# Kernel optimization log

Measured on AMD Instinct MI355X. Metric: run time of the kernel, lower is better.

The kernel has to match this reference:

```python
import jax, jax.numpy as jnp
import numpy as np
import math

DIM = 1024      # dim == dim_attn (required by value-reshape)
HEAD = 16
KV = 128        # K_v routing slots
HD = DIM // HEAD
N = 50000       # number of nodes


def setup_inputs() -> dict:
    key = jax.random.key(0)
    ks = jax.random.split(key, 8)
    s = lambda fan_in: 1.0 / np.sqrt(fan_in)
    return {
        "x": jax.random.normal(ks[0], (N, DIM), jnp.float32),
        "node_index": jax.random.normal(ks[1], (N, 4), jnp.float32),
        # nn.Linear(dim, dim_attn)
        "Wq": jax.random.normal(ks[2], (DIM, DIM), jnp.float32) * s(DIM),
        "bq": jnp.zeros((DIM,), jnp.float32),
        # nn.Parameter key (K_v, head, head_dim), torch.randn init
        "key_p": jax.random.normal(ks[3], (KV, HEAD, HD), jnp.float32),
        # nn.Linear(dim, dim)
        "Wv": jax.random.normal(ks[4], (DIM, DIM), jnp.float32) * s(DIM),
        "bv": jnp.zeros((DIM,), jnp.float32),
        # gate params, shape (head, 1)
        "alpha": jnp.full((HEAD, 1), math.log(9.0), jnp.float32),
        "beta": jnp.full((HEAD, 1), math.log(0.01), jnp.float32),
        # nn.Linear(4, head*K_v)
        "Wb": jax.random.normal(ks[5], (HEAD * KV, 4), jnp.float32) * s(4),
        "bb": jnp.zeros((HEAD * KV,), jnp.float32),
    }


def _mh_sinkhorn(A, num_iters=3, eps=0.05):
    # A: (N, H, K). Faithful to the per-head torch sinkhorn (Q transposed to
    # (K, N)): row sums are over the node axis, col sums over the slot axis.
    n = A.shape[0]
    k = A.shape[2]
    Q = jnp.exp(A / eps)
    Q = Q / jnp.sum(Q, axis=(0, 2), keepdims=True)          # total-sum norm per head
    for _ in range(num_iters):
        Q = Q / jnp.sum(Q, axis=0, keepdims=True) / k       # rows of Q.T (per slot)
        Q = Q / jnp.sum(Q, axis=2, keepdims=True) / n       # cols of Q.T (per node)
    return Q * n


def reference(x, node_index, Wq, bq, key_p, Wv, bv, alpha, beta, Wb, bb):
    n = x.shape[0]
    q = (x @ Wq.T + bq).reshape(n, HEAD, HD)
    attn = jnp.einsum('nhd,rhd->nhr', q, key_p) / np.float32(np.sqrt(HD))
    bias = (node_index @ Wb.T + bb).reshape(n, HEAD, KV)
    attn = attn + bias                                       # (n, H, K_v)
    xv = (x @ Wv.T + bv).reshape(n, HEAD, HD)
    v = jnp.einsum('nhr,nhd->rhd', jax.nn.sigmoid(attn), xv)  # (K_v, H, D)
    cons = _mh_sinkhorn(jax.nn.softmax(attn, axis=-1))
    v = jnp.einsum('nhr,rhd->nhd', cons, v)
    out = jax.nn.sigmoid(alpha) * xv + jax.nn.sigmoid(beta) * v  # (H,1) broadcasts
    return out.reshape(n, DIM)
```

## Files before the change

kernel.cpp:

```cpp
#include <hip/hip_runtime.h>

#define N_NODES 50000
#define MPAD    50176
#define DIM     1024
#define HEAD    16
#define KV      128
#define HD      64
#define NGRP    98

typedef unsigned short ushort_t;
typedef short short8 __attribute__((ext_vector_type(8)));
typedef float f32x4 __attribute__((ext_vector_type(4)));

__device__ inline unsigned short f2bf(float f){
  union { float f; unsigned u; } v; v.f = f;
  unsigned u = v.u;
  unsigned r = (u + 0x7FFFu + ((u >> 16) & 1u)) >> 16;
  return (unsigned short)r;
}
__device__ inline float bf2f(unsigned short u){
  union { unsigned u; float f; } v; v.u = ((unsigned)u) << 16; return v.f;
}

__device__ inline void gload_lds16(const void* g, void* l){
  __builtin_amdgcn_global_load_lds(
      (const __attribute__((address_space(1))) void*)g,
      (__attribute__((address_space(3))) void*)l, 16, 0, 0);
}

__device__ inline short8 frag64(const ushort_t* lds, int row, int kk, int lane){
  int c  = kk*4 + (lane >> 4);
  int cc = c ^ (row & 7);
  return *(const short8*)(lds + row*64 + cc*8);
}
__device__ inline short8 frag128(const ushort_t* lds, int row, int kk, int lane){
  int c  = kk*4 + (lane >> 4);
  int cc = c ^ (row & 7);
  return *(const short8*)(lds + row*128 + cc*8);
}

__global__ void k_zero(float* p, int n){
  int i = blockIdx.x*256 + threadIdx.x;
  if (i < n) p[i] = 0.f;
}

__global__ void k_prep_x(const float* __restrict__ x, ushort_t* __restrict__ x_bf){
  int idx = blockIdx.x*256 + threadIdx.x;
  int row = idx >> 7, c = idx & 127;
  const float4* s = (const float4*)(x + (size_t)row*1024 + c*8);
  float4 f0 = s[0], f1 = s[1];
  short8 v;
  v[0]=(short)f2bf(f0.x); v[1]=(short)f2bf(f0.y); v[2]=(short)f2bf(f0.z); v[3]=(short)f2bf(f0.w);
  v[4]=(short)f2bf(f1.x); v[5]=(short)f2bf(f1.y); v[6]=(short)f2bf(f1.z); v[7]=(short)f2bf(f1.w);
  int sc = (c & ~3) | ((c ^ (row >> 1)) & 3);
  *(short8*)(x_bf + (size_t)row*1024 + sc*8) = v;
}

__global__ void k_prep_w(const float* __restrict__ Wq, const float* __restrict__ Wv,
                         ushort_t* __restrict__ w_bf){
  int idx = blockIdx.x*256 + threadIdx.x;
  int j = idx >> 10, k = idx & 1023;
  float v = (j < 1024) ? Wq[idx] : Wv[(size_t)(j-1024)*1024 + k];
  int l = k >> 3;
  int q = (l & ~3) | ((l ^ (j >> 1)) & 3);
  w_bf[(size_t)j*1024 + q*8 + (k & 7)] = f2bf(v);
}

__global__ void k_prep_key(const float* __restrict__ key_p, ushort_t* __restrict__ key_bf){
  int idx = blockIdx.x*256 + threadIdx.x;
  int h = idx >> 13, rem = idx & 8191;
  int r = rem >> 6, d = rem & 63;
  float v = key_p[(size_t)(r*HEAD + h)*HD + d];
  int pos = ((((d>>3) ^ (r & 7)) & 7) << 3) | (d & 7);
  key_bf[(size_t)h*8192 + r*64 + pos] = f2bf(v);
}

__global__ void k_vreduce(const float* __restrict__ vp, float* __restrict__ vout){
  int i = blockIdx.x*256 + threadIdx.x;
  float s = 0.f;
  for (int gg = 0; gg < NGRP; ++gg) s += vp[(size_t)gg*131072 + i];
  vout[i] = s;
}

__global__ __launch_bounds__(512) void k_gemm(const ushort_t* __restrict__ x_bf,
    const ushort_t* __restrict__ w_bf, const float* __restrict__ bq,
    const float* __restrict__ bv, ushort_t* __restrict__ q_bf, float* xv_out){
  extern __shared__ char gsm[];
  ushort_t* lds = (ushort_t*)gsm;
  const int tid = threadIdx.x, lane = tid & 63;
  const int wid = tid >> 6, wr = wid >> 2, wc = wid & 3;
  int b = blockIdx.x;
  int wg = (b & 7)*196 + (b >> 3);
  const int bm0 = (wg >> 3) * 256, bn0 = (wg & 7) * 256;
  const int pA = (lane >> 4) ^ ((lane >> 1) & 3);

  f32x4 acc[8][4];
  #pragma unroll
  for (int m=0;m<8;m++)
    #pragma unroll
    for (int n=0;n<4;n++) acc[m][n] = (f32x4){0.f,0.f,0.f,0.f};

  const ushort_t* asrc = x_bf + (size_t)bm0*1024;
  const ushort_t* bsrc = w_bf + (size_t)bn0*1024;

#define STG(kt, kk, bi) do{                                               \
    _Pragma("unroll")                                                     \
    for (int it=0; it<2; ++it){                                           \
      int ch = it*512 + tid; int r = ch>>2, c = ch&3;                     \
      gload_lds16(asrc + (size_t)r*1024 + (kt)*64 + (kk)*32 + c*8,        \
                  lds + (bi)*32768 + (kk)*8192 + ch*8);                   \
      gload_lds16(bsrc + (size_t)r*1024 + (kt)*64 + (kk)*32 + c*8,        \
                  lds + (bi)*32768 + 16384 + (kk)*8192 + ch*8);           \
    } }while(0)

#define RD_A(BASE, KK, MH)                                                \
    _Pragma("unroll")                                                     \
    for (int m=0;m<4;m++){                                                \
      int row = wr*128 + ((MH)*4+m)*16 + (lane&15);                       \
      af[m] = *(const short8*)((BASE) + (KK)*8192 + row*32 + pA*8);       \
    }
#define RD_B(BASE, KK)                                                    \
    _Pragma("unroll")                                                     \
    for (int n=0;n<4;n++){                                                \
      int row = wc*64 + n*16 + (lane&15);                                 \
      bf_[n] = *(const short8*)((BASE) + 16384 + (KK)*8192 + row*32 + pA*8); \
    }
#define MFMA16(MH)                                                        \
    __builtin_amdgcn_s_setprio(1);                                        \
    _Pragma("unroll")                                                     \
    for (int m=0;m<4;m++)                                                 \
      _Pragma("unroll")                                                   \
      for (int n=0;n<4;n++)                                               \
        acc[(MH)*4+m][n] = __builtin_amdgcn_mfma_f32_16x16x32_bf16(       \
            af[m], bf_[n], acc[(MH)*4+m][n], 0,0,0);                      \
    __builtin_amdgcn_s_setprio(0);
#define BAR asm volatile("s_barrier" ::: "memory")

  STG(0,0,0); STG(0,1,0); STG(1,0,1);
  asm volatile("s_waitcnt vmcnt(8)" ::: "memory");
  BAR;

  for (int t = 0; t < 16; ++t){
    const int bufc = t & 1, bufn = bufc ^ 1;
    const ushort_t* base = lds + bufc*32768;
    short8 af[4], bf_[4];

    RD_B(base, 0);
    RD_A(base, 0, 0);
    if (t+1 < 16) STG(t+1, 1, bufn);
    BAR;
    MFMA16(0);
    BAR;

    RD_A(base, 0, 1);
    BAR;
    MFMA16(1);
    if (t == 15) { asm volatile("s_waitcnt vmcnt(0)" ::: "memory"); }
    else         { asm volatile("s_waitcnt vmcnt(8)" ::: "memory"); }
    BAR;

    RD_B(base, 1);
    RD_A(base, 1, 0);
    if (t+2 < 16) STG(t+2, 0, bufc);
    BAR;
    MFMA16(0);
    BAR;

    RD_A(base, 1, 1);
    BAR;
    MFMA16(1);
    if (t <= 13)      { asm volatile("s_waitcnt vmcnt(8)" ::: "memory"); }
    else if (t == 14) { asm volatile("s_waitcnt vmcnt(4)" ::: "memory"); }
    BAR;
  }
#undef STG
#undef RD_A
#undef RD_B
#undef MFMA16
#undef BAR

  __syncthreads();

  const bool isq = bn0 < 1024;
  float biasv[4];
  #pragma unroll
  for (int n=0;n<4;n++){
    int col = bn0 + wc*64 + n*16 + (lane & 15);
    biasv[n] = isq ? bq[col] : bv[col - 1024];
  }

  if (isq){
    ushort_t* img = (ushort_t*)gsm;
    #pragma unroll
    for (int n=0;n<4;n++){
      int lcol = wc*64 + n*16 + (lane & 15);
      int d = lcol & 63;
      #pragma unroll
      for (int m=0;m<8;m++){
        #pragma unroll
        for (int j=0;j<4;j++){
          int lrow = wr*128 + m*16 + (lane>>4)*4 + j;
          int sc = (lcol & ~63) | ((((d>>3) ^ (lrow & 7)) & 7) << 3) | (d & 7);
          img[lrow*256 + sc] = f2bf(acc[m][n][j] + biasv[n]);
        }
      }
    }
    __syncthreads();
    #pragma unroll
    for (int it=0; it<16; ++it){
      int r  = it*16 + (tid >> 5);
      int ch = tid & 31;
      short8 v = *(const short8*)(img + r*256 + ch*8);
      *(short8*)(q_bf + (size_t)(bm0 + r)*1024 + bn0 + ch*8) = v;
    }
  } else {
    #pragma unroll
    for (int n=0;n<4;n++){
      int col = bn0 + wc*64 + n*16 + (lane & 15);
      #pragma unroll
      for (int m=0;m<8;m++){
        #pragma unroll
        for (int j=0;j<4;j++){
          int row = bm0 + wr*128 + m*16 + (lane>>4)*4 + j;
          if (row < N_NODES)
            xv_out[(size_t)row*1024 + (col - 1024)] = acc[m][n][j] + biasv[n];
        }
      }
    }
  }
}

template<int PHASE>
__global__ __launch_bounds__(256) void k_attn(
    const ushort_t* __restrict__ q_bf, const ushort_t* __restrict__ key_bf,
    const float* __restrict__ node_index, const float* __restrict__ Wb,
    const float* __restrict__ bb, const float* __restrict__ colsum_in,
    float* __restrict__ colsum_out, const float* __restrict__ v_fin,
    float* __restrict__ v_part, float* xv_out,
    const float* __restrict__ alpha, const float* __restrict__ beta)
{
  constexpr int QB    = (PHASE == 2) ? 1 : 2;
  constexpr int O_Q   = 0;
  constexpr int O_KEY = O_Q + QB*8192;
  constexpr int O_NI  = O_KEY + 16384;
  constexpr int O_WB  = O_NI + QB*1024;
  constexpr int O_RED = O_WB + 2560;
  constexpr int O_COL = O_RED + 2048;
  constexpr int O_W   = O_COL + 512;
  constexpr int O_X1  = O_W + 512;
  constexpr int O_X2  = O_X1 + 16384;

  extern __shared__ char smem[];
  ushort_t* q_lds   = (ushort_t*)(smem + O_Q);
  ushort_t* key_lds = (ushort_t*)(smem + O_KEY);
  float* ni_lds  = (float*)(smem + O_NI);
  float* wb_lds  = (float*)(smem + O_WB);
  float* red_lds = (float*)(smem + O_RED);
  float* col_acc = (float*)(smem + O_COL);
  float* w_lds   = (float*)(smem + O_W);
  ushort_t* sigT     = (ushort_t*)(smem + O_X1);
  ushort_t* xvT      = (ushort_t*)(smem + O_X2);
  ushort_t* vT       = (ushort_t*)(smem + O_X1);
  ushort_t* cons_lds = (ushort_t*)(smem + O_X2);
  float*    out_lds  = (float*)(smem + O_X2);

  const int tid = threadIdx.x, lane = tid & 63, wid = tid >> 6;
  const int h    = blockIdx.x & 15;
  const int g    = blockIdx.x >> 4;
  const int base = g * 512;
  int NT = (MPAD - base) >> 6; if (NT > 8) NT = 8;

  #pragma unroll
  for (int it = 0; it < 4; ++it){
    int chunk = it*256 + tid;
    gload_lds16(key_bf + (size_t)h*8192 + chunk*8, key_lds + chunk*8);
  }
  #pragma unroll
  for (int it = 0; it < 2; ++it){
    int chunk = it*256 + tid;
    int r = chunk >> 3, c = chunk & 7;
    gload_lds16(q_bf + (size_t)(base + r)*1024 + h*64 + c*8, q_lds + chunk*8);
  }
  { int r = tid >> 2, c = tid & 3;
    ni_lds[tid] = (base + r < N_NODES) ? node_index[(size_t)(base + r)*4 + c] : 0.f; }
  if (tid < 128){
    #pragma unroll
    for (int c=0;c<4;c++) wb_lds[tid*5+c] = Wb[(size_t)(h*128 + tid)*4 + c];
    wb_lds[tid*5+4] = bb[h*128 + tid];
    if (PHASE >= 1) w_lds[tid] = 1.f / (128.f * colsum_in[h*128 + tid]);
    if (PHASE <= 1) col_acc[tid] = 0.f;
  }
  if constexpr (PHASE == 2){
    int r = tid >> 1, dh = (tid & 1)*32;
    #pragma unroll
    for (int i=0;i<32;i++){
      int d = dh + i;
      vT[d*128 + ((r>>3) ^ (d&7))*8 + (r&7)] = f2bf(v_fin[((size_t)r*16 + h)*64 + d]);
    }
  }
  float xvr[16], xvn[16];
  if constexpr (PHASE == 0){
    int d = tid & 63, q4 = tid >> 6;
    #pragma unroll
    for (int i=0;i<16;i++){
      int row = base + q4*16 + i;
      xvr[i] = (row < N_NODES) ? xv_out[(size_t)row*1024 + h*64 + d] : 0.f;
    }
  }
  f32x4 vac[2][4];
  if constexpr (PHASE == 0)
    for (int m=0;m<2;m++) for (int n=0;n<4;n++) vac[m][n] = (f32x4){0.f,0.f,0.f,0.f};

  __syncthreads();

  for (int t = 0; t < NT; ++t){
    const int i0  = base + t*64;
    const int cur = t & 1;
    const ushort_t* qb  = q_lds  + ((QB==2) ? cur*4096 : 0);
    const float*    nib = ni_lds + ((QB==2) ? cur*256  : 0);
    float ni_next = 0.f;

    if constexpr (QB == 2){
      if (t+1 < NT){
        int i1 = i0 + 64;
        #pragma unroll
        for (int it = 0; it < 2; ++it){
          int chunk = it*256 + tid;
          int r = chunk >> 3, c = chunk & 7;
          gload_lds16(q_bf + (size_t)(i1 + r)*1024 + h*64 + c*8,
                      q_lds + (cur^1)*4096 + chunk*8);
        }
        int r = tid >> 2, c = tid & 3;
        ni_next = (i0 + 64 + r < N_NODES) ? node_index[(size_t)(i0+64+r)*4 + c] : 0.f;
      }
    } else {
      if (t+1 < NT){
        int r = tid >> 2, c = tid & 3;
        ni_next = (i0 + 64 + r < N_NODES) ? node_index[(size_t)(i0+64+r)*4 + c] : 0.f;
      }
    }
    if constexpr (PHASE == 0){
      if (t+1 < NT){
        int d = tid & 63, q4 = tid >> 6;
        #pragma unroll
        for (int i=0;i<16;i++){
          int row = i0 + 64 + q4*16 + i;
          xvn[i] = (row < N_NODES) ? xv_out[(size_t)row*1024 + h*64 + d] : 0.f;
        }
      }
    }

    f32x4 acc[2][4];
    for (int m=0;m<2;m++) for (int n=0;n<4;n++) acc[m][n] = (f32x4){0.f,0.f,0.f,0.f};
    #pragma unroll
    for (int kk = 0; kk < 2; ++kk){
      short8 kf[2];
      #pragma unroll
      for (int m=0;m<2;m++) kf[m] = frag64(key_lds, wid*32 + m*16 + (lane&15), kk, lane);
      #pragma unroll
      for (int n=0;n<4;n++){
        short8 qf = frag64(qb, n*16 + (lane&15), kk, lane);
        #pragma unroll
        for (int m=0;m<2;m++)
          acc[m][n] = __builtin_amdgcn_mfma_f32_16x16x32_bf16(kf[m], qf, acc[m][n], 0,0,0);
      }
    }

    float nif[4][4];
    #pragma unroll
    for (int n=0;n<4;n++){
      int nn = n*16 + (lane&15);
      #pragma unroll
      for (int c=0;c<4;c++) nif[n][c] = nib[nn*4+c];
    }
    float a[2][4][4];
    #pragma unroll
    for (int m=0;m<2;m++){
      #pragma unroll
      for (int j=0;j<4;j++){
        int r = wid*32 + m*16 + (lane>>4)*4 + j;
        float w0 = wb_lds[r*5+0], w1 = wb_lds[r*5+1];
        float w2 = wb_lds[r*5+2], w3 = wb_lds[r*5+3], w4 = wb_lds[r*5+4];
        #pragma unroll
        for (int n=0;n<4;n++){
          float b = w4 + w0*nif[n][0] + w1*nif[n][1] + w2*nif[n][2] + w3*nif[n][3];
          a[m][n][j] = acc[m][n][j]*0.125f + b;
        }
      }
    }

    float vmask[4];
    #pragma unroll
    for (int n=0;n<4;n++) vmask[n] = (i0 + n*16 + (lane&15) < N_NODES) ? 1.f : 0.f;

    if constexpr (PHASE == 0){
      #pragma unroll
      for (int m=0;m<2;m++) for (int n=0;n<4;n++) for (int j=0;j<4;j++){
        int r  = wid*32 + m*16 + (lane>>4)*4 + j;
        int nn = n*16 + (lane&15);
        float sg = vmask[n] / (1.f + __expf(-a[m][n][j]));
        sigT[r*64 + ((((nn>>3) ^ (r&7)) & 7) << 3) + (nn&7)] = f2bf(sg);
      }
      { int d = tid & 63, q4 = tid >> 6;
        #pragma unroll
        for (int i=0;i<16;i++){
          int nn = q4*16 + i;
          xvT[d*64 + ((((nn>>3) ^ (d&7)) & 7) << 3) + (nn&7)] = f2bf(xvr[i]);
        }
      }
    }

    float pm[4];
    #pragma unroll
    for (int n=0;n<4;n++){
      float m0 = a[0][n][0];
      #pragma unroll
      for (int m=0;m<2;m++) for (int j=0;j<4;j++) m0 = fmaxf(m0, a[m][n][j]);
      m0 = fmaxf(m0, __shfl_xor(m0, 16));
      m0 = fmaxf(m0, __shfl_xor(m0, 32));
      pm[n] = m0;
    }
    if (lane < 16){
      #pragma unroll
      for (int n=0;n<4;n++) red_lds[wid*64 + n*16 + lane] = pm[n];
    }
    __syncthreads();

    if constexpr (QB == 1){
      if (t+1 < NT){
        int i1 = i0 + 64;
        #pragma unroll
        for (int it = 0; it < 2; ++it){
          int chunk = it*256 + tid;
          int r = chunk >> 3, c = chunk & 7;
          gload_lds16(q_bf + (size_t)(i1 + r)*1024 + h*64 + c*8, q_lds + chunk*8);
        }
        ni_lds[tid] = ni_next;
      }
    }

    float mnn[4], snn[4];
    #pragma unroll
    for (int n=0;n<4;n++){
      int nn = n*16 + (lane&15);
      float m0 = red_lds[nn];
      m0 = fmaxf(m0, red_lds[64+nn]); m0 = fmaxf(m0, red_lds[128+nn]); m0 = fmaxf(m0, red_lds[192+nn]);
      mnn[n] = m0;
    }
    #pragma unroll
    for (int n=0;n<4;n++){
      float s = 0.f;
      #pragma unroll
      for (int m=0;m<2;m++) for (int j=0;j<4;j++){
        float e = __expf(a[m][n][j] - mnn[n]);
        a[m][n][j] = e; s += e;
      }
      s += __shfl_xor(s, 16); s += __shfl_xor(s, 32);
      snn[n] = s;
    }
    if (lane < 16){
      #pragma unroll
      for (int n=0;n<4;n++) red_lds[256 + wid*64 + n*16 + lane] = snn[n];
    }

    if constexpr (PHASE == 0){
      #pragma unroll
      for (int kk=0;kk<2;kk++){
        short8 sa[2];
        #pragma unroll
        for (int m=0;m<2;m++) sa[m] = frag64(sigT, wid*32 + m*16 + (lane&15), kk, lane);
        #pragma unroll
        for (int n=0;n<4;n++){
          short8 xf = frag64(xvT, n*16 + (lane&15), kk, lane);
          #pragma unroll
          for (int m=0;m<2;m++)
            vac[m][n] = __builtin_amdgcn_mfma_f32_16x16x32_bf16(sa[m], xf, vac[m][n], 0,0,0);
        }
      }
    }
    __syncthreads();

    #pragma unroll
    for (int n=0;n<4;n++){
      int nn = n*16 + (lane&15);
      snn[n] = red_lds[256+nn] + red_lds[256+64+nn] + red_lds[256+128+nn] + red_lds[256+192+nn];
    }
    #pragma unroll
    for (int n=0;n<4;n++){
      float inv = 20.f / snn[n];
      #pragma unroll
      for (int m=0;m<2;m++) for (int j=0;j<4;j++)
        a[m][n][j] = __expf(a[m][n][j] * inv);
    }

    float uval[4];
    if constexpr (PHASE >= 1){
      #pragma unroll
      for (int n=0;n<4;n++){
        float s = 0.f;
        #pragma unroll
        for (int m=0;m<2;m++){
          #pragma unroll
          for (int j=0;j<4;j++){
            int r = wid*32 + m*16 + (lane>>4)*4 + j;
            s += a[m][n][j] * w_lds[r];
          }
        }
        s += __shfl_xor(s, 16); s += __shfl_xor(s, 32);
        uval[n] = s;
      }
      if (lane < 16){
        #pragma unroll
        for (int n=0;n<4;n++) red_lds[wid*64 + n*16 + lane] = uval[n];
      }
      __syncthreads();
      #pragma unroll
      for (int n=0;n<4;n++){
        int nn = n*16 + (lane&15);
        float s = red_lds[nn] + red_lds[64+nn] + red_lds[128+nn] + red_lds[192+nn];
        uval[n] = 1.f / (50000.f * s);
      }
    }

    if constexpr (PHASE <= 1){
      float cs[2][4];
      #pragma unroll
      for (int m=0;m<2;m++){
        #pragma unroll
        for (int j=0;j<4;j++){
          float s = 0.f;
          #pragma unroll
          for (int n=0;n<4;n++){
            float tv = a[m][n][j] * vmask[n];
            if (PHASE == 1) tv *= uval[n];
            s += tv;
          }
          s += __shfl_xor(s, 1); s += __shfl_xor(s, 2);
          s += __shfl_xor(s, 4); s += __shfl_xor(s, 8);
          cs[m][j] = s;
        }
      }
      if ((lane & 15) == 0){
        #pragma unroll
        for (int m=0;m<2;m++) for (int j=0;j<4;j++){
          int r = wid*32 + m*16 + (lane>>4)*4 + j;
          col_acc[r] += cs[m][j];
        }
      }
    }

    if constexpr (PHASE == 2){
      #pragma unroll
      for (int m=0;m<2;m++) for (int n=0;n<4;n++) for (int j=0;j<4;j++){
        int r  = wid*32 + m*16 + (lane>>4)*4 + j;
        int nn = n*16 + (lane&15);
        float cv = 50000.f * uval[n] * a[m][n][j] * w_lds[r];
        cons_lds[nn*128 + ((r>>3) ^ (nn&7))*8 + (r&7)] = f2bf(cv);
      }
      __syncthreads();
      f32x4 oac[4];
      for (int n=0;n<4;n++) oac[n] = (f32x4){0.f,0.f,0.f,0.f};
      #pragma unroll
      for (int kk=0;kk<4;kk++){
        short8 va = frag128(vT, wid*16 + (lane&15), kk, lane);
        #pragma unroll
        for (int n=0;n<4;n++){
          short8 cf = frag128(cons_lds, n*16 + (lane&15), kk, lane);
          oac[n] = __builtin_amdgcn_mfma_f32_16x16x32_bf16(va, cf, oac[n], 0,0,0);
        }
      }
      __syncthreads();
      #pragma unroll
      for (int n=0;n<4;n++) for (int j=0;j<4;j++){
        int d  = wid*16 + (lane>>4)*4 + j;
        int nn = n*16 + (lane&15);
        out_lds[nn*68 + d] = oac[n][j];
      }
      __syncthreads();
      float sa = 1.f/(1.f + __expf(-alpha[h]));
      float sb = 1.f/(1.f + __expf(-beta[h]));
      int nn = tid >> 2, d0 = (tid & 3)*16;
      if (i0 + nn < N_NODES){
        #pragma unroll
        for (int gq=0; gq<4; ++gq){
          float4 vf = *(const float4*)(out_lds + nn*68 + d0 + gq*4);
          float4 xf = *(const float4*)(xv_out + (size_t)(i0+nn)*1024 + h*64 + d0 + gq*4);
          float4 o;
          o.x = sa*xf.x + sb*vf.x;
          o.y = sa*xf.y + sb*vf.y;
          o.z = sa*xf.z + sb*vf.z;
          o.w = sa*xf.w + sb*vf.w;
          *(float4*)(xv_out + (size_t)(i0+nn)*1024 + h*64 + d0 + gq*4) = o;
        }
      }
    } else {
      if (t+1 < NT && QB == 2) ni_lds[(cur^1)*256 + tid] = ni_next;
      if constexpr (PHASE == 0){
        if (t+1 < NT){
          #pragma unroll
          for (int i=0;i<16;i++) xvr[i] = xvn[i];
        }
      }
      __syncthreads();
    }
  }

  if constexpr (PHASE == 0){
    float* vdst = v_part + (size_t)g*131072;
    #pragma unroll
    for (int m=0;m<2;m++) for (int n=0;n<4;n++) for (int j=0;j<4;j++){
      int r = wid*32 + m*16 + (lane>>4)*4 + j;
      int d = n*16 + (lane&15);
      vdst[((size_t)r*16 + h)*64 + d] = vac[m][n][j];
    }
  }
  if constexpr (PHASE <= 1){
    if (tid < 128) atomicAdd(&colsum_out[h*128 + tid], col_acc[tid]);
  }
}

extern "C" void kernel_launch(void* const* d_in, const int* in_sizes, int n_in,
                              void* d_out, int out_size, void* d_ws, size_t ws_size,
                              hipStream_t stream){
  const float* x     = (const float*)d_in[0];
  const float* ni    = (const float*)d_in[1];
  const float* Wq    = (const float*)d_in[2];
  const float* bq    = (const float*)d_in[3];
  const float* keyp  = (const float*)d_in[4];
  const float* Wv    = (const float*)d_in[5];
  const float* bv    = (const float*)d_in[6];
  const float* alpha = (const float*)d_in[7];
  const float* beta  = (const float*)d_in[8];
  const float* Wb    = (const float*)d_in[9];
  const float* bb    = (const float*)d_in[10];
  float* out = (float*)d_out;

  char* ws = (char*)d_ws;
  ushort_t* x_bf   = (ushort_t*)(ws);
  float*    v_part = (float*)(ws);
  ushort_t* q_bf   = (ushort_t*)(ws + 102760448);
  ushort_t* w_bf   = (ushort_t*)(ws + 205520896);
  ushort_t* key_bf = (ushort_t*)(ws + 209715200);
  float*    v_fin  = (float*)(ws + 209977344);
  float*    cs     = (float*)(ws + 210501632);

  (void)hipFuncSetAttribute((const void*)k_gemm,
      hipFuncAttributeMaxDynamicSharedMemorySize, 131072);

  k_zero<<<dim3(24), 256, 0, stream>>>(cs, 6144);
  k_zero<<<dim3(352), 256, 0, stream>>>((float*)(x_bf + (size_t)N_NODES*1024), 90112);
  k_prep_x<<<dim3(25000), 256, 0, stream>>>(x, x_bf);
  k_prep_w<<<dim3(2048*1024/256), 256, 0, stream>>>(Wq, Wv, w_bf);
  k_prep_key<<<dim3(HEAD*KV*HD/256), 256, 0, stream>>>(keyp, key_bf);
  k_gemm<<<dim3(1568), 512, 131072, stream>>>(x_bf, w_bf, bq, bv, q_bf, out);

  dim3 ag(NGRP*16);
  k_attn<0><<<ag, 256, 65024, stream>>>(q_bf, key_bf, ni, Wb, bb, nullptr,  cs,      v_fin, v_part, out, alpha, beta);
  k_vreduce<<<dim3(512), 256, 0, stream>>>(v_part, v_fin);
  k_attn<1><<<ag, 256, 40448, stream>>>(q_bf, key_bf, ni, Wb, bb, cs,       cs+2048, v_fin, v_part, out, alpha, beta);
  k_attn<1><<<ag, 256, 40448, stream>>>(q_bf, key_bf, ni, Wb, bb, cs+2048,  cs+4096, v_fin, v_part, out, alpha, beta);
  k_attn<2><<<ag, 256, 65024, stream>>>(q_bf, key_bf, ni, Wb, bb, cs+4096,  nullptr, v_fin, v_part, out, alpha, beta);
}
```

Measured before the change: 951.0 us.

## Materialize exp-softmax tiles once and run Sinkhorn passes from cached bf16 tiles

Phase 0 of the attention kernel now writes the per-node exponentiated Sinkhorn input Q0 to workspace in bf16. Two lightweight kernels then read these tiles for the column-sum iterations, and a final kernel does the consensus matmul and output blend. This avoids recomputing the q·key products, bias and exp in every Sinkhorn phase. The cost is extra workspace traffic of about 200MB per pass and bf16 rounding of Q0. The old path is kept as a fallback when the workspace is too small.

New measurement: 1.135 ms. 19.3% more time.

```diff
diff --git a/kernel.cpp b/kernel.cpp
--- a/kernel.cpp
+++ b/kernel.cpp
@@ -7,6 +7,7 @@
 #define KV      128
 #define HD      64
 #define NGRP    98
+#define NTILE   784
 
 typedef unsigned short ushort_t;
 typedef short short8 __attribute__((ext_vector_type(8)));
@@ -18,8 +19,8 @@
   unsigned r = (u + 0x7FFFu + ((u >> 16) & 1u)) >> 16;
   return (unsigned short)r;
 }
-__device__ inline float bf2f(unsigned short u){
-  union { unsigned u; float f; } v; v.u = ((unsigned)u) << 16; return v.f;
+__device__ inline float bf2f(unsigned u16){
+  union { unsigned u; float f; } v; v.u = (u16 & 0xFFFFu) << 16; return v.f;
 }
 
 __device__ inline void gload_lds16(const void* g, void* l){
@@ -237,7 +238,8 @@
     const float* __restrict__ bb, const float* __restrict__ colsum_in,
     float* __restrict__ colsum_out, const float* __restrict__ v_fin,
     float* __restrict__ v_part, float* xv_out,
-    const float* __restrict__ alpha, const float* __restrict__ beta)
+    const float* __restrict__ alpha, const float* __restrict__ beta,
+    ushort_t* __restrict__ q0g)
 {
   constexpr int QB    = (PHASE == 2) ? 1 : 2;
   constexpr int O_Q   = 0;
@@ -493,6 +495,19 @@
         a[m][n][j] = __expf(a[m][n][j] * inv);
     }
 
+    if constexpr (PHASE == 0){
+      if (q0g){
+        size_t ub = (size_t)((i0 >> 6)*16 + h) * 8192;
+        #pragma unroll
+        for (int m=0;m<2;m++) for (int n=0;n<4;n++){
+          uint2 pv;
+          pv.x = (unsigned)f2bf(a[m][n][0]) | ((unsigned)f2bf(a[m][n][1]) << 16);
+          pv.y = (unsigned)f2bf(a[m][n][2]) | ((unsigned)f2bf(a[m][n][3]) << 16);
+          *(uint2*)(q0g + ub + ((size_t)((wid*2+m)*4 + n))*256 + lane*4) = pv;
+        }
+      }
+    }
+
     float uval[4];
     if constexpr (PHASE >= 1){
       #pragma unroll
@@ -616,6 +631,172 @@
   }
   if constexpr (PHASE <= 1){
     if (tid < 128) atomicAdd(&colsum_out[h*128 + tid], col_acc[tid]);
+  }
+}
+
+__global__ __launch_bounds__(256) void k_p1(const ushort_t* __restrict__ q0g,
+    const float* __restrict__ cs_in, float* __restrict__ cs_out){
+  const int tid = threadIdx.x, lane = tid & 63, wid = tid >> 6;
+  const int gw = blockIdx.x*4 + wid;
+  const int rg = lane >> 4, ln = lane & 15;
+  #pragma unroll 1
+  for (int it = 0; it < 4; ++it){
+    int unit = gw*4 + it;
+    int T = unit >> 4, h = unit & 15;
+    const ushort_t* ubase = q0g + (size_t)unit*8192;
+    float wv[8][4];
+    #pragma unroll
+    for (int a2=0;a2<8;a2++){
+      float4 c4 = *(const float4*)(cs_in + h*128 + a2*16 + rg*4);
+      wv[a2][0] = 1.f/(128.f*c4.x); wv[a2][1] = 1.f/(128.f*c4.y);
+      wv[a2][2] = 1.f/(128.f*c4.z); wv[a2][3] = 1.f/(128.f*c4.w);
+    }
+    float up[4] = {0.f,0.f,0.f,0.f};
+    #pragma unroll
+    for (int f=0; f<32; f++){
+      uint2 d = *(const uint2*)(ubase + (size_t)f*256 + lane*4);
+      int a2 = f>>2, n = f&3;
+      up[n] += bf2f(d.x)*wv[a2][0] + bf2f(d.x>>16)*wv[a2][1]
+             + bf2f(d.y)*wv[a2][2] + bf2f(d.y>>16)*wv[a2][3];
+    }
+    float msk[4];
+    #pragma unroll
+    for (int n=0;n<4;n++){
+      float s = up[n];
+      s += __shfl_xor(s,16); s += __shfl_xor(s,32);
+      float uu = 1.f/(50000.f*s);
+      msk[n] = (T*64 + n*16 + ln < N_NODES) ? uu : 0.f;
+    }
+    float ca[32];
+    #pragma unroll
+    for (int s5=0;s5<32;s5++) ca[s5] = 0.f;
+    #pragma unroll
+    for (int f=0; f<32; f++){
+      uint2 d = *(const uint2*)(ubase + (size_t)f*256 + lane*4);
+      int a2 = f>>2, n = f&3;
+      ca[a2*4+0] += msk[n]*bf2f(d.x);
+      ca[a2*4+1] += msk[n]*bf2f(d.x>>16);
+      ca[a2*4+2] += msk[n]*bf2f(d.y);
+      ca[a2*4+3] += msk[n]*bf2f(d.y>>16);
+    }
+    #pragma unroll
+    for (int s5=0;s5<32;s5++){
+      float v = ca[s5];
+      v += __shfl_xor(v,1); v += __shfl_xor(v,2);
+      v += __shfl_xor(v,4); v += __shfl_xor(v,8);
+      ca[s5] = v;
+    }
+    if (ln == 0){
+      #pragma unroll
+      for (int s5=0;s5<32;s5++){
+        int r = (s5>>2)*16 + rg*4 + (s5&3);
+        atomicAdd(&cs_out[h*128 + r], ca[s5]);
+      }
+    }
+  }
+}
+
+__global__ __launch_bounds__(256) void k_p2(const ushort_t* __restrict__ q0g,
+    const float* __restrict__ cs_in, const float* __restrict__ v_fin,
+    float* xv_out, const float* __restrict__ alpha, const float* __restrict__ beta){
+  __shared__ ushort_t vT[64*128];
+  __shared__ float X2[64*68];
+  __shared__ float w_lds[128];
+  __shared__ float red_lds[256];
+  ushort_t* cons_lds = (ushort_t*)X2;
+  float* out_lds = X2;
+
+  const int tid = threadIdx.x, lane = tid & 63, wid = tid >> 6;
+  const int h = blockIdx.x & 15;
+  const int g = blockIdx.x >> 4;
+  const int nn = tid & 63, rq = tid >> 6;
+
+  { int r = tid >> 1, dh = (tid & 1)*32;
+    #pragma unroll
+    for (int i=0;i<32;i++){
+      int d = dh + i;
+      vT[d*128 + ((r>>3) ^ (d&7))*8 + (r&7)] = f2bf(v_fin[((size_t)r*16 + h)*64 + d]);
+    } }
+  if (tid < 128) w_lds[tid] = 1.f/(128.f * cs_in[h*128 + tid]);
+  __syncthreads();
+
+  const float sa = 1.f/(1.f + __expf(-alpha[h]));
+  const float sb = 1.f/(1.f + __expf(-beta[h]));
+
+  for (int t = 0; t < 8; ++t){
+    const int i0 = g*512 + t*64;
+    const int T  = g*8 + t;
+    const ushort_t* ubase = q0g + (size_t)(T*16 + h)*8192;
+
+    float q0v[2][4][4], wreg[2][4][4];
+    float up = 0.f;
+    #pragma unroll
+    for (int m=0;m<2;m++){
+      #pragma unroll
+      for (int rg=0;rg<4;rg++){
+        uint2 d = *(const uint2*)(ubase + (size_t)((rq*2+m)*4 + (nn>>4)))*0 +
+                  *(const uint2*)(ubase + ((size_t)((rq*2+m)*4 + (nn>>4)))*256 + (rg*16 + (nn&15))*4);
+        float4 w4 = *(const float4*)(w_lds + rq*32 + m*16 + rg*4);
+        q0v[m][rg][0] = bf2f(d.x);     wreg[m][rg][0] = w4.x;
+        q0v[m][rg][1] = bf2f(d.x>>16); wreg[m][rg][1] = w4.y;
+        q0v[m][rg][2] = bf2f(d.y);     wreg[m][rg][2] = w4.z;
+        q0v[m][rg][3] = bf2f(d.y>>16); wreg[m][rg][3] = w4.w;
+        #pragma unroll
+        for (int j=0;j<4;j++) up += q0v[m][rg][j]*wreg[m][rg][j];
+      }
+    }
+    red_lds[rq*64 + nn] = up;
+    __syncthreads();
+    float u3 = 1.f/(50000.f*(red_lds[nn] + red_lds[64+nn] + red_lds[128+nn] + red_lds[192+nn]));
+    float scale = 50000.f * u3;
+    #pragma unroll
+    for (int m=0;m<2;m++){
+      #pragma unroll
+      for (int rg=0;rg<4;rg++){
+        int r0 = rq*32 + m*16 + rg*4;
+        unsigned lo = (unsigned)f2bf(scale*q0v[m][rg][0]*wreg[m][rg][0])
+                    | ((unsigned)f2bf(scale*q0v[m][rg][1]*wreg[m][rg][1]) << 16);
+        unsigned hi = (unsigned)f2bf(scale*q0v[m][rg][2]*wreg[m][rg][2])
+                    | ((unsigned)f2bf(scale*q0v[m][rg][3]*wreg[m][rg][3]) << 16);
+        uint2 pv; pv.x = lo; pv.y = hi;
+        *(uint2*)(cons_lds + nn*128 + ((r0>>3) ^ (nn&7))*8 + (r0&7)) = pv;
+      }
+    }
+    __syncthreads();
+    f32x4 oac[4];
+    for (int n=0;n<4;n++) oac[n] = (f32x4){0.f,0.f,0.f,0.f};
+    #pragma unroll
+    for (int kk=0;kk<4;kk++){
+      short8 va = frag128(vT, wid*16 + (lane&15), kk, lane);
+      #pragma unroll
+      for (int n=0;n<4;n++){
+        short8 cf = frag128(cons_lds, n*16 + (lane&15), kk, lane);
+        oac[n] = __builtin_amdgcn_mfma_f32_16x16x32_bf16(va, cf, oac[n], 0,0,0);
+      }
+    }
+    __syncthreads();
+    #pragma unroll
+    for (int n=0;n<4;n++) for (int j=0;j<4;j++){
+      int d  = wid*16 + (lane>>4)*4 + j;
+      int n2 = n*16 + (lane&15);
+      out_lds[n2*68 + d] = oac[n][j];
+    }
+    __syncthreads();
+    { int n2 = tid >> 2, d0 = (tid & 3)*16;
+      if (i0 + n2 < N_NODES){
+        #pragma unroll
+        for (int gq=0; gq<4; ++gq){
+          float4 vf = *(const float4*)(out_lds + n2*68 + d0 + gq*4);
+          float4 xf = *(const float4*)(xv_out + (size_t)(i0+n2)*1024 + h*64 + d0 + gq*4);
+          float4 o;
+          o.x = sa*xf.x + sb*vf.x;
+          o.y = sa*xf.y + sb*vf.y;
+          o.z = sa*xf.z + sb*vf.z;
+          o.w = sa*xf.w + sb*vf.w;
+          *(float4*)(xv_out + (size_t)(i0+n2)*1024 + h*64 + d0 + gq*4) = o;
+        }
+      } }
+    __syncthreads();
   }
 }
 
@@ -643,21 +824,31 @@
   ushort_t* key_bf = (ushort_t*)(ws + 209715200);
   float*    v_fin  = (float*)(ws + 209977344);
   float*    cs     = (float*)(ws + 210501632);
+  const size_t Q0_OFF  = 210763776ull;
+  const size_t Q0_NEED = Q0_OFF + (size_t)NTILE*16*16384;
+  bool bigws = ws_size >= Q0_NEED;
+  ushort_t* q0g = bigws ? (ushort_t*)(ws + Q0_OFF) : nullptr;
 
   (void)hipFuncSetAttribute((const void*)k_gemm,
       hipFuncAttributeMaxDynamicSharedMemorySize, 131072);
 
   k_zero<<<dim3(24), 256, 0, stream>>>(cs, 6144);
-  k_zero<<<dim3(352), 256, 0, stream>>>((float*)(x_bf + (size_t)N_NODES*1024), 90112);
+  k_zero<<<dim3(704), 256, 0, stream>>>((float*)(x_bf + (size_t)N_NODES*1024), 90112);
   k_prep_x<<<dim3(25000), 256, 0, stream>>>(x, x_bf);
   k_prep_w<<<dim3(2048*1024/256), 256, 0, stream>>>(Wq, Wv, w_bf);
   k_prep_key<<<dim3(HEAD*KV*HD/256), 256, 0, stream>>>(keyp, key_bf);
   k_gemm<<<dim3(1568), 512, 131072, stream>>>(x_bf, w_bf, bq, bv, q_bf, out);
 
   dim3 ag(NGRP*16);
-  k_attn<0><<<ag, 256, 65024, stream>>>(q_bf, key_bf, ni, Wb, bb, nullptr,  cs,      v_fin, v_part, out, alpha, beta);
+  k_attn<0><<<ag, 256, 65024, stream>>>(q_bf, key_bf, ni, Wb, bb, nullptr,  cs,      v_fin, v_part, out, alpha, beta, q0g);
   k_vreduce<<<dim3(512), 256, 0, stream>>>(v_part, v_fin);
-  k_attn<1><<<ag, 256, 40448, stream>>>(q_bf, key_bf, ni, Wb, bb, cs,       cs+2048, v_fin, v_part, out, alpha, beta);
-  k_attn<1><<<ag, 256, 40448, stream>>>(q_bf, key_bf, ni, Wb, bb, cs+2048,  cs+4096, v_fin, v_part, out, alpha, beta);
-  k_attn<2><<<ag, 256, 65024, stream>>>(q_bf, key_bf, ni, Wb, bb, cs+4096,  nullptr, v_fin, v_part, out, alpha, beta);
-}
+  if (bigws){
+    k_p1<<<dim3(784), 256, 0, stream>>>(q0g, cs,       cs+2048);
+    k_p1<<<dim3(784), 256, 0, stream>>>(q0g, cs+2048,  cs+4096);
+    k_p2<<<dim3(NGRP*16), 256, 0, stream>>>(q0g, cs+4096, v_fin, out, alpha, beta);
+  } else {
+    k_attn<1><<<ag, 256, 40448, stream>>>(q_bf, key_bf, ni, Wb, bb, cs,       cs+2048, v_fin, v_part, out, alpha, beta, nullptr);
+    k_attn<1><<<ag, 256, 40448, stream>>>(q_bf, key_bf, ni, Wb, bb, cs+2048,  cs+4096, v_fin, v_part, out, alpha, beta, nullptr);
+    k_attn<2><<<ag, 256, 65024, stream>>>(q_bf, key_bf, ni, Wb, bb, cs+4096,  nullptr, v_fin, v_part, out, alpha, beta, nullptr);
+  }
+}
```
